# Optimization experiments

Measured on AMD Instinct MI355X. Metric: run time of the kernel, lower is better.

## Reference

```python
import jax, jax.numpy as jnp
import numpy as np

N = 100_000      # nodes
E = 3_200_000    # edges (avg degree 32)
F_IN = 64        # num_node_features
G = 256          # graphs in batch


def _lin(key, fan_in, fan_out):
    kw, kb = jax.random.split(key)
    bound = 1.0 / np.sqrt(fan_in)
    W = jax.random.uniform(kw, (fan_in, fan_out), jnp.float32, -bound, bound)
    b = jax.random.uniform(kb, (fan_out,), jnp.float32, -bound, bound)
    return W, b


def setup_inputs() -> dict:
    key = jax.random.key(0)
    ks = jax.random.split(key, 9)
    x = jax.random.normal(ks[0], (N, F_IN), jnp.float32)
    edge_index = jax.random.randint(ks[1], (2, E), 0, N, dtype=jnp.int64)
    batch = jnp.sort(jax.random.randint(ks[2], (N,), 0, G, dtype=jnp.int64))
    W1, b1 = _lin(ks[3], F_IN, 60)
    W2, b2 = _lin(ks[4], 60, 50)
    Wf1, bf1 = _lin(ks[5], 50, 30)
    Wf2, bf2 = _lin(ks[6], 30, 20)
    Wf3, bf3 = _lin(ks[7], 20, 10)
    Wo, bo = _lin(ks[8], 10, 1)
    return {"x": x, "edge_index": edge_index, "batch": batch,
            "W1": W1, "b1": b1, "W2": W2, "b2": b2,
            "Wf1": Wf1, "bf1": bf1, "Wf2": Wf2, "bf2": bf2,
            "Wf3": Wf3, "bf3": bf3, "Wo": Wo, "bo": bo}


def _gcn_norm(edge_index, n_nodes):
    # add self loops, then symmetric D^{-1/2} (A+I) D^{-1/2} edge weights
    loop = jnp.arange(n_nodes, dtype=edge_index.dtype)
    src = jnp.concatenate([edge_index[0], loop])
    dst = jnp.concatenate([edge_index[1], loop])
    deg = jax.ops.segment_sum(jnp.ones_like(dst, dtype=jnp.float32), dst,
                              num_segments=n_nodes)
    dinv = jax.lax.rsqrt(deg)  # deg >= 1 thanks to self loops
    norm = dinv[src] * dinv[dst]
    return src, dst, norm


def _gcn_conv(h, W, b, src, dst, norm, n_nodes):
    h = h @ W                                            # [N, out]
    msg = h[src] * norm[:, None]                         # gather over edges
    agg = jax.ops.segment_sum(msg, dst, num_segments=n_nodes)
    return agg + b


def reference(x, edge_index, batch, W1, b1, W2, b2,
              Wf1, bf1, Wf2, bf2, Wf3, bf3, Wo, bo):
    n_nodes = x.shape[0]
    src, dst, norm = _gcn_norm(edge_index, n_nodes)
    h = _gcn_conv(x, W1, b1, src, dst, norm, n_nodes)    # [N, 60]
    h = _gcn_conv(h, W2, b2, src, dst, norm, n_nodes)    # [N, 50]
    # global_add_pool over graph ids
    g = jax.ops.segment_sum(h, batch, num_segments=G)    # [G, 50]
    # MLP stack (no nonlinearities in the original forward)
    g = g @ Wf1 + bf1
    g = g @ Wf2 + bf2
    g = g @ Wf3 + bf3
    return g @ Wo + bo                                   # [G, 1]
```

## Files before the change

kernel.cpp:

```cpp
#include <hip/hip_runtime.h>


#define RSHIFT 7
#define RNODES 128
#define NB_MAX 1024
#define NBLK 512
#define STHREADS 512
#define STAGE_CAP 8192

__global__ void collapse_weights_k(
    const float* __restrict__ W1, const float* __restrict__ b1,
    const float* __restrict__ W2, const float* __restrict__ b2,
    const float* __restrict__ Wf1, const float* __restrict__ bf1,
    const float* __restrict__ Wf2, const float* __restrict__ bf2,
    const float* __restrict__ Wf3, const float* __restrict__ bf3,
    const float* __restrict__ Wo, const float* __restrict__ bo,
    float* __restrict__ w1c, float* __restrict__ sc)
{
    __shared__ float wo[10], w3[20], w2[30], w1[50], w2c[60];
    const int t = threadIdx.x;
    if (t < 10) wo[t] = Wo[t];
    __syncthreads();
    if (t < 20) { float s = 0.f; for (int j = 0; j < 10; ++j) s += Wf3[t*10+j]*wo[j]; w3[t] = s; }
    __syncthreads();
    if (t < 30) { float s = 0.f; for (int j = 0; j < 20; ++j) s += Wf2[t*20+j]*w3[j]; w2[t] = s; }
    __syncthreads();
    if (t < 50) { float s = 0.f; for (int j = 0; j < 30; ++j) s += Wf1[t*30+j]*w2[j]; w1[t] = s; }
    __syncthreads();
    if (t < 60) { float s = 0.f; for (int j = 0; j < 50; ++j) s += W2[t*50+j]*w1[j]; w2c[t] = s; }
    __syncthreads();
    { float s = 0.f; for (int j = 0; j < 60; ++j) s += W1[t*60+j]*w2c[j]; w1c[t] = s; }
    if (t == 0) {
        float c1 = 0.f; for (int j = 0; j < 60; ++j) c1 += b1[j]*w2c[j];
        float c2 = 0.f; for (int j = 0; j < 50; ++j) c2 += b2[j]*w1[j];
        float c0 = bo[0];
        for (int j = 0; j < 30; ++j) c0 += bf1[j]*w2[j];
        for (int j = 0; j < 20; ++j) c0 += bf2[j]*w3[j];
        for (int j = 0; j < 10; ++j) c0 += bf3[j]*wo[j];
        sc[0] = c1; sc[1] = c2; sc[2] = c0;
    }
}

__global__ void node_u_k(const float* __restrict__ x, const float* __restrict__ w1c,
                         float* __restrict__ u, int n) {
    int tid = blockIdx.x * blockDim.x + threadIdx.x;
    int wave = tid >> 6;
    int lane = threadIdx.x & 63;
    int node = wave * 4 + (lane >> 4);
    int sub = lane & 15;
    if (node >= n) return;
    float4 xv = *reinterpret_cast<const float4*>(x + (size_t)node * 64 + sub * 4);
    float4 wv = *reinterpret_cast<const float4*>(w1c + sub * 4);
    float val = xv.x * wv.x + xv.y * wv.y + xv.z * wv.z + xv.w * wv.w;
    val += __shfl_down(val, 8, 16);
    val += __shfl_down(val, 4, 16);
    val += __shfl_down(val, 2, 16);
    val += __shfl_down(val, 1, 16);
    if (sub == 0) u[node] = val;
}

__global__ void bin_count_k(const int* __restrict__ dst, int E, int chunk,
                            int nb, int* __restrict__ cnt_bm) {
    __shared__ int hist[NB_MAX];
    int tid = threadIdx.x;
    hist[tid] = 0; hist[tid + 512] = 0;
    __syncthreads();
    int e0 = blockIdx.x * chunk;
    int e1 = e0 + chunk; if (e1 > E) e1 = E;
    for (int j = 0; j < STAGE_CAP / (STHREADS * 4); ++j) {
        int i = e0 + tid * 4 + j * (STHREADS * 4);
        if (i + 3 < e1) {
            int4 d = *reinterpret_cast<const int4*>(dst + i);
            atomicAdd(&hist[d.x >> RSHIFT], 1);
            atomicAdd(&hist[d.y >> RSHIFT], 1);
            atomicAdd(&hist[d.z >> RSHIFT], 1);
            atomicAdd(&hist[d.w >> RSHIFT], 1);
        } else if (i < e1) {
            for (int k = i; k < e1; ++k) atomicAdd(&hist[dst[k] >> RSHIFT], 1);
        }
    }
    __syncthreads();
    for (int b = tid; b < nb; b += STHREADS)
        cnt_bm[(size_t)blockIdx.x * nb + b] = hist[b];
}

__global__ void scanA_k(const int* __restrict__ cnt_bm, int nb,
                        int* __restrict__ offs, int* __restrict__ total) {
    __shared__ int sums[STHREADS];
    int k = threadIdx.x, b = blockIdx.x;
    int v = cnt_bm[(size_t)k * nb + b];
    sums[k] = v;
    __syncthreads();
    for (int off = 1; off < STHREADS; off <<= 1) {
        int a = (k >= off) ? sums[k - off] : 0;
        __syncthreads();
        sums[k] += a;
        __syncthreads();
    }
    offs[(size_t)b * NBLK + k] = sums[k] - v;
    if (k == STHREADS - 1) total[b] = sums[k];
}

__global__ void scanB_k(const int* __restrict__ total, int nb,
                        int* __restrict__ base, int* __restrict__ endp,
                        const float* __restrict__ sc, float* __restrict__ out, int G) {
    __shared__ int sums[STHREADS];
    int t = threadIdx.x;
    if (t < G) out[t] = sc[2];
    int b0 = 2 * t, b1 = 2 * t + 1;
    int t0 = (b0 < nb) ? total[b0] : 0;
    int t1 = (b1 < nb) ? total[b1] : 0;
    int a0 = (t0 + 3) & ~3, a1 = (t1 + 3) & ~3;
    int pair = a0 + a1;
    sums[t] = pair;
    __syncthreads();
    for (int off = 1; off < STHREADS; off <<= 1) {
        int a = (t >= off) ? sums[t - off] : 0;
        __syncthreads();
        sums[t] += a;
        __syncthreads();
    }
    int excl = sums[t] - pair;
    if (b0 < nb) { base[b0] = excl; endp[b0] = excl + t0; }
    if (b1 < nb) { base[b1] = excl + a0; endp[b1] = excl + a0 + t1; }
}

__global__ void bin_scatter_k(const int* __restrict__ src, const int* __restrict__ dst,
                              int E, int chunk, int nb,
                              const int* __restrict__ base, const int* __restrict__ offs,
                              unsigned int* __restrict__ binned) {
    __shared__ int hist[NB_MAX];
    __shared__ int tbase[NB_MAX];
    __shared__ int adj[NB_MAX];
    __shared__ int sums[STHREADS];
    __shared__ unsigned int staged[STAGE_CAP];
    __shared__ unsigned short bof[STAGE_CAP];
    const int tid = threadIdx.x;
    hist[tid] = 0; hist[tid + 512] = 0;
    __syncthreads();
    int e0 = blockIdx.x * chunk;
    int e1 = e0 + chunk; if (e1 > E) e1 = E;
    const int QMAX = STAGE_CAP / (STHREADS * 4);
    unsigned int pk[QMAX * 4];
    int bk[QMAX * 4];
    int rk[QMAX * 4];
    int nv[QMAX];
    #pragma unroll
    for (int j = 0; j < QMAX; ++j) {
        int i = e0 + tid * 4 + j * (STHREADS * 4);
        int cnt = e1 - i; if (cnt > 4) cnt = 4; if (cnt < 0) cnt = 0;
        nv[j] = cnt;
        if (cnt == 4) {
            int4 s4 = *reinterpret_cast<const int4*>(src + i);
            int4 d4 = *reinterpret_cast<const int4*>(dst + i);
            pk[j*4+0] = (unsigned)s4.x | ((unsigned)(d4.x & (RNODES-1)) << 17);
            pk[j*4+1] = (unsigned)s4.y | ((unsigned)(d4.y & (RNODES-1)) << 17);
            pk[j*4+2] = (unsigned)s4.z | ((unsigned)(d4.z & (RNODES-1)) << 17);
            pk[j*4+3] = (unsigned)s4.w | ((unsigned)(d4.w & (RNODES-1)) << 17);
            bk[j*4+0] = d4.x >> RSHIFT; bk[j*4+1] = d4.y >> RSHIFT;
            bk[j*4+2] = d4.z >> RSHIFT; bk[j*4+3] = d4.w >> RSHIFT;
            rk[j*4+0] = atomicAdd(&hist[bk[j*4+0]], 1);
            rk[j*4+1] = atomicAdd(&hist[bk[j*4+1]], 1);
            rk[j*4+2] = atomicAdd(&hist[bk[j*4+2]], 1);
            rk[j*4+3] = atomicAdd(&hist[bk[j*4+3]], 1);
        } else {
            for (int l = 0; l < cnt; ++l) {
                int s = src[i + l], d = dst[i + l];
                pk[j*4+l] = (unsigned)s | ((unsigned)(d & (RNODES-1)) << 17);
                bk[j*4+l] = d >> RSHIFT;
                rk[j*4+l] = atomicAdd(&hist[bk[j*4+l]], 1);
            }
        }
    }
    __syncthreads();
    int h0 = hist[2*tid], h1 = hist[2*tid+1];
    int pair = h0 + h1;
    sums[tid] = pair;
    __syncthreads();
    for (int off = 1; off < STHREADS; off <<= 1) {
        int a = (tid >= off) ? sums[tid - off] : 0;
        __syncthreads();
        sums[tid] += a;
        __syncthreads();
    }
    int excl = sums[tid] - pair;
    tbase[2*tid] = excl;
    tbase[2*tid+1] = excl + h0;
    for (int b = 2*tid; b <= 2*tid+1; ++b)
        if (b < nb) adj[b] = base[b] + offs[(size_t)b * NBLK + blockIdx.x] - tbase[b];
    __syncthreads();
    #pragma unroll
    for (int j = 0; j < QMAX; ++j) {
        for (int l = 0; l < nv[j]; ++l) {
            int b = bk[j*4+l];
            int slot = tbase[b] + rk[j*4+l];
            staged[slot] = pk[j*4+l];
            bof[slot] = (unsigned short)b;
        }
    }
    __syncthreads();
    int tcount = e1 - e0;
    for (int s = tid; s < tcount; s += STHREADS) {
        int b = bof[s];
        binned[adj[b] + s] = staged[s];
    }
}

__global__ void degree_k(const unsigned int* __restrict__ binned, const int* __restrict__ base,
                         const int* __restrict__ endp, const float* __restrict__ u,
                         float* __restrict__ dinv, float* __restrict__ w, int n) {
    __shared__ int cnt[RNODES];
    int tid = threadIdx.x, b = blockIdx.x;
    if (tid < RNODES) cnt[tid] = 0;
    __syncthreads();
    int s0 = base[b], s1 = endp[b];
    int nvec = (s1 - s0) >> 2;
    for (int k = tid; k < nvec; k += blockDim.x) {
        uint4 p = *reinterpret_cast<const uint4*>(binned + s0 + 4 * k);
        atomicAdd(&cnt[p.x >> 17], 1);
        atomicAdd(&cnt[p.y >> 17], 1);
        atomicAdd(&cnt[p.z >> 17], 1);
        atomicAdd(&cnt[p.w >> 17], 1);
    }
    int i = s0 + 4 * nvec + tid;
    if (i < s1) atomicAdd(&cnt[binned[i] >> 17], 1);
    __syncthreads();
    int g = (b << RSHIFT) + tid;
    if (tid < RNODES && g < n) {
        float d = rsqrtf((float)(cnt[tid] + 1));
        dinv[g] = d;
        w[g] = d * u[g];
    }
}

__global__ void conv_mid_k(const unsigned int* __restrict__ binned, const int* __restrict__ base,
                           const int* __restrict__ endp,
                           const float* __restrict__ w, const float* __restrict__ dinv,
                           const float* __restrict__ u, const float* __restrict__ sc,
                           float* __restrict__ v, float* __restrict__ wb, int n) {
    __shared__ float acc[RNODES];
    int tid = threadIdx.x, b = blockIdx.x;
    if (tid < RNODES) acc[tid] = 0.f;
    __syncthreads();
    int s0 = base[b], s1 = endp[b];
    int nvec = (s1 - s0) >> 2;
    for (int k = tid; k < nvec; k += blockDim.x) {
        uint4 p = *reinterpret_cast<const uint4*>(binned + s0 + 4 * k);
        float wx = w[p.x & 0x1FFFF];
        float wy = w[p.y & 0x1FFFF];
        float wz = w[p.z & 0x1FFFF];
        float ww = w[p.w & 0x1FFFF];
        atomicAdd(&acc[p.x >> 17], wx);
        atomicAdd(&acc[p.y >> 17], wy);
        atomicAdd(&acc[p.z >> 17], wz);
        atomicAdd(&acc[p.w >> 17], ww);
    }
    int i = s0 + 4 * nvec + tid;
    if (i < s1) { unsigned p = binned[i]; atomicAdd(&acc[p >> 17], w[p & 0x1FFFF]); }
    __syncthreads();
    int g = (b << RSHIFT) + tid;
    if (tid < RNODES && g < n) {
        float di = dinv[g];
        float val = sc[0] + di * acc[tid] + di * di * u[g];
        v[g] = val;
        wb[g] = di * val;
    }
}

__global__ void conv_final_k(const unsigned int* __restrict__ binned, const int* __restrict__ base,
                             const int* __restrict__ endp,
                             const float* __restrict__ wb, const float* __restrict__ dinv,
                             const float* __restrict__ v, const float* __restrict__ sc,
                             const int* __restrict__ batch, float* __restrict__ out, int n) {
    __shared__ float acc[RNODES];
    __shared__ float tbuf[RNODES];
    __shared__ int gbuf[RNODES];
    int tid = threadIdx.x, b = blockIdx.x;
    if (tid < RNODES) acc[tid] = 0.f;
    __syncthreads();
    int s0 = base[b], s1 = endp[b];
    int nvec = (s1 - s0) >> 2;
    for (int k = tid; k < nvec; k += blockDim.x) {
        uint4 p = *reinterpret_cast<const uint4*>(binned + s0 + 4 * k);
        float wx = wb[p.x & 0x1FFFF];
        float wy = wb[p.y & 0x1FFFF];
        float wz = wb[p.z & 0x1FFFF];
        float ww = wb[p.w & 0x1FFFF];
        atomicAdd(&acc[p.x >> 17], wx);
        atomicAdd(&acc[p.y >> 17], wy);
        atomicAdd(&acc[p.z >> 17], wz);
        atomicAdd(&acc[p.w >> 17], ww);
    }
    int i = s0 + 4 * nvec + tid;
    if (i < s1) { unsigned p = binned[i]; atomicAdd(&acc[p >> 17], wb[p & 0x1FFFF]); }
    __syncthreads();
    int g = (b << RSHIFT) + tid;
    float tval = 0.f; int gid = -1;
    if (tid < RNODES && g < n) {
        float di = dinv[g];
        tval = sc[1] + di * acc[tid] + di * di * v[g];
        gid = batch[g];
    }
    if (tid < RNODES) { tbuf[tid] = tval; gbuf[tid] = gid; }
    __syncthreads();
    if (tid < RNODES && g < n) {
        bool head = (tid == 0) || (gbuf[tid - 1] != gid);
        if (head) {
            float s = 0.f;
            int i2 = tid;
            while (i2 < RNODES && gbuf[i2] == gid) { s += tbuf[i2]; ++i2; }
            atomicAdd(&out[gid], s);
        }
    }
}

extern "C" void kernel_launch(void* const* d_in, const int* in_sizes, int n_in,
                              void* d_out, int out_size, void* d_ws, size_t ws_size,
                              hipStream_t stream)
{
    const float* x    = (const float*)d_in[0];
    const int*   ei   = (const int*)d_in[1];
    const int*   batch= (const int*)d_in[2];
    const float* W1   = (const float*)d_in[3];
    const float* b1   = (const float*)d_in[4];
    const float* W2   = (const float*)d_in[5];
    const float* b2   = (const float*)d_in[6];
    const float* Wf1  = (const float*)d_in[7];
    const float* bf1  = (const float*)d_in[8];
    const float* Wf2  = (const float*)d_in[9];
    const float* bf2  = (const float*)d_in[10];
    const float* Wf3  = (const float*)d_in[11];
    const float* bf3  = (const float*)d_in[12];
    const float* Wo   = (const float*)d_in[13];
    const float* bo   = (const float*)d_in[14];
    float* out = (float*)d_out;

    const int n = in_sizes[0] / 64;
    const int E = in_sizes[1] / 2;
    const int G = out_size;
    const int* src = ei;
    const int* dst = ei + E;
    const int nb = (n + RNODES - 1) >> RSHIFT;

    float* ws_f = (float*)d_ws;
    int*   ws_i = (int*)d_ws;
    float* w1c    = ws_f;
    float* sc     = ws_f + 64;
    int*   basep  = ws_i + 128;
    int*   endp   = ws_i + 128 + NB_MAX;
    int*   total  = ws_i + 128 + 2*NB_MAX;
    int*   offs   = ws_i + 128 + 3*NB_MAX;
    size_t off_u  = 128 + 3*(size_t)NB_MAX + (size_t)nb * NBLK;
    off_u = (off_u + 3) & ~(size_t)3;
    float* u      = ws_f + off_u;
    float* dinv   = u + n;
    float* w      = dinv + n;
    float* v      = w + n;
    float* wb     = v + n;
    size_t off_b  = off_u + 5*(size_t)n;
    off_b = (off_b + 3) & ~(size_t)3;
    unsigned int* binned = (unsigned int*)(ws_f + off_b);
    int* cnt_bm = (int*)binned;

    int chunk = (E + NBLK - 1) / NBLK;
    chunk = (chunk + 3) & ~3;

    hipLaunchKernelGGL(collapse_weights_k, dim3(1), dim3(64), 0, stream,
                       W1, b1, W2, b2, Wf1, bf1, Wf2, bf2, Wf3, bf3, Wo, bo, w1c, sc);
    hipLaunchKernelGGL(node_u_k, dim3((n / 4 * 64 + 255) / 256 + 1), dim3(256), 0, stream,
                       x, w1c, u, n);
    hipLaunchKernelGGL(bin_count_k, dim3(NBLK), dim3(STHREADS), 0, stream,
                       dst, E, chunk, nb, cnt_bm);
    hipLaunchKernelGGL(scanA_k, dim3(nb), dim3(STHREADS), 0, stream,
                       cnt_bm, nb, offs, total);
    hipLaunchKernelGGL(scanB_k, dim3(1), dim3(STHREADS), 0, stream,
                       total, nb, basep, endp, sc, out, G);
    hipLaunchKernelGGL(bin_scatter_k, dim3(NBLK), dim3(STHREADS), 0, stream,
                       src, dst, E, chunk, nb, basep, offs, binned);
    hipLaunchKernelGGL(degree_k, dim3(nb), dim3(512), 0, stream,
                       binned, basep, endp, u, dinv, w, n);
    hipLaunchKernelGGL(conv_mid_k, dim3(nb), dim3(512), 0, stream,
                       binned, basep, endp, w, dinv, u, sc, v, wb, n);
    hipLaunchKernelGGL(conv_final_k, dim3(nb), dim3(512), 0, stream,
                       binned, basep, endp, wb, dinv, v, sc, batch, out, n);
}
```

Before: 204.4 us.

## Replace counting-sort passes with fixed-capacity bins and atomic cursors

Removes the separate bin-count pass and the two scan kernels by giving each destination bin a fixed capacity slot (BCAP) and reserving space with global atomic cursors in the scatter kernel. Node degrees are now computed with global atomics during scatter, replacing the degree pass over binned edges with a simple elementwise dinv kernel. This cuts a full read of dst and several launches, at the cost of global atomic contention and the assumption that no bin exceeds BCAP edges, which holds for uniform random graphs but would overflow on skewed degree distributions.

New measurement: 320.9 us. 1.57x slower.

```diff
diff --git a/kernel.cpp b/kernel.cpp
--- a/kernel.cpp
+++ b/kernel.cpp
@@ -7,6 +7,7 @@
 #define NBLK 512
 #define STHREADS 512
 #define STAGE_CAP 8192
+#define BCAP 6144
 
 __global__ void collapse_weights_k(
     const float* __restrict__ W1, const float* __restrict__ b1,
@@ -15,10 +16,12 @@
     const float* __restrict__ Wf2, const float* __restrict__ bf2,
     const float* __restrict__ Wf3, const float* __restrict__ bf3,
     const float* __restrict__ Wo, const float* __restrict__ bo,
-    float* __restrict__ w1c, float* __restrict__ sc)
+    float* __restrict__ w1c, float* __restrict__ sc,
+    int* __restrict__ cursor)
 {
     __shared__ float wo[10], w3[20], w2[30], w1[50], w2c[60];
     const int t = threadIdx.x;
+    for (int b = t; b < NB_MAX; b += 64) cursor[b] = 0;
     if (t < 10) wo[t] = Wo[t];
     __syncthreads();
     if (t < 20) { float s = 0.f; for (int j = 0; j < 10; ++j) s += Wf3[t*10+j]*wo[j]; w3[t] = s; }
@@ -42,13 +45,14 @@
 }
 
 __global__ void node_u_k(const float* __restrict__ x, const float* __restrict__ w1c,
-                         float* __restrict__ u, int n) {
+                         float* __restrict__ u, int* __restrict__ deg, int n) {
     int tid = blockIdx.x * blockDim.x + threadIdx.x;
     int wave = tid >> 6;
     int lane = threadIdx.x & 63;
     int node = wave * 4 + (lane >> 4);
     int sub = lane & 15;
     if (node >= n) return;
+    if (sub == 1) deg[node] = 0;
     float4 xv = *reinterpret_cast<const float4*>(x + (size_t)node * 64 + sub * 4);
     float4 wv = *reinterpret_cast<const float4*>(w1c + sub * 4);
     float val = xv.x * wv.x + xv.y * wv.y + xv.z * wv.z + xv.w * wv.w;
@@ -59,76 +63,10 @@
     if (sub == 0) u[node] = val;
 }
 
-__global__ void bin_count_k(const int* __restrict__ dst, int E, int chunk,
-                            int nb, int* __restrict__ cnt_bm) {
-    __shared__ int hist[NB_MAX];
-    int tid = threadIdx.x;
-    hist[tid] = 0; hist[tid + 512] = 0;
-    __syncthreads();
-    int e0 = blockIdx.x * chunk;
-    int e1 = e0 + chunk; if (e1 > E) e1 = E;
-    for (int j = 0; j < STAGE_CAP / (STHREADS * 4); ++j) {
-        int i = e0 + tid * 4 + j * (STHREADS * 4);
-        if (i + 3 < e1) {
-            int4 d = *reinterpret_cast<const int4*>(dst + i);
-            atomicAdd(&hist[d.x >> RSHIFT], 1);
-            atomicAdd(&hist[d.y >> RSHIFT], 1);
-            atomicAdd(&hist[d.z >> RSHIFT], 1);
-            atomicAdd(&hist[d.w >> RSHIFT], 1);
-        } else if (i < e1) {
-            for (int k = i; k < e1; ++k) atomicAdd(&hist[dst[k] >> RSHIFT], 1);
-        }
-    }
-    __syncthreads();
-    for (int b = tid; b < nb; b += STHREADS)
-        cnt_bm[(size_t)blockIdx.x * nb + b] = hist[b];
-}
-
-__global__ void scanA_k(const int* __restrict__ cnt_bm, int nb,
-                        int* __restrict__ offs, int* __restrict__ total) {
-    __shared__ int sums[STHREADS];
-    int k = threadIdx.x, b = blockIdx.x;
-    int v = cnt_bm[(size_t)k * nb + b];
-    sums[k] = v;
-    __syncthreads();
-    for (int off = 1; off < STHREADS; off <<= 1) {
-        int a = (k >= off) ? sums[k - off] : 0;
-        __syncthreads();
-        sums[k] += a;
-        __syncthreads();
-    }
-    offs[(size_t)b * NBLK + k] = sums[k] - v;
-    if (k == STHREADS - 1) total[b] = sums[k];
-}
-
-__global__ void scanB_k(const int* __restrict__ total, int nb,
-                        int* __restrict__ base, int* __restrict__ endp,
-                        const float* __restrict__ sc, float* __restrict__ out, int G) {
-    __shared__ int sums[STHREADS];
-    int t = threadIdx.x;
-    if (t < G) out[t] = sc[2];
-    int b0 = 2 * t, b1 = 2 * t + 1;
-    int t0 = (b0 < nb) ? total[b0] : 0;
-    int t1 = (b1 < nb) ? total[b1] : 0;
-    int a0 = (t0 + 3) & ~3, a1 = (t1 + 3) & ~3;
-    int pair = a0 + a1;
-    sums[t] = pair;
-    __syncthreads();
-    for (int off = 1; off < STHREADS; off <<= 1) {
-        int a = (t >= off) ? sums[t - off] : 0;
-        __syncthreads();
-        sums[t] += a;
-        __syncthreads();
-    }
-    int excl = sums[t] - pair;
-    if (b0 < nb) { base[b0] = excl; endp[b0] = excl + t0; }
-    if (b1 < nb) { base[b1] = excl + a0; endp[b1] = excl + a0 + t1; }
-}
-
-__global__ void bin_scatter_k(const int* __restrict__ src, const int* __restrict__ dst,
-                              int E, int chunk, int nb,
-                              const int* __restrict__ base, const int* __restrict__ offs,
-                              unsigned int* __restrict__ binned) {
+__global__ void scatter_k(const int* __restrict__ src, const int* __restrict__ dst,
+                          int E, int chunk, int nb,
+                          int* __restrict__ cursor, int* __restrict__ deg,
+                          unsigned int* __restrict__ binned) {
     __shared__ int hist[NB_MAX];
     __shared__ int tbase[NB_MAX];
     __shared__ int adj[NB_MAX];
@@ -153,6 +91,10 @@
         if (cnt == 4) {
             int4 s4 = *reinterpret_cast<const int4*>(src + i);
             int4 d4 = *reinterpret_cast<const int4*>(dst + i);
+            atomicAdd(&deg[d4.x], 1);
+            atomicAdd(&deg[d4.y], 1);
+            atomicAdd(&deg[d4.z], 1);
+            atomicAdd(&deg[d4.w], 1);
             pk[j*4+0] = (unsigned)s4.x | ((unsigned)(d4.x & (RNODES-1)) << 17);
             pk[j*4+1] = (unsigned)s4.y | ((unsigned)(d4.y & (RNODES-1)) << 17);
             pk[j*4+2] = (unsigned)s4.z | ((unsigned)(d4.z & (RNODES-1)) << 17);
@@ -166,6 +108,7 @@
         } else {
             for (int l = 0; l < cnt; ++l) {
                 int s = src[i + l], d = dst[i + l];
+                atomicAdd(&deg[d], 1);
                 pk[j*4+l] = (unsigned)s | ((unsigned)(d & (RNODES-1)) << 17);
                 bk[j*4+l] = d >> RSHIFT;
                 rk[j*4+l] = atomicAdd(&hist[bk[j*4+l]], 1);
@@ -186,8 +129,17 @@
     int excl = sums[tid] - pair;
     tbase[2*tid] = excl;
     tbase[2*tid+1] = excl + h0;
-    for (int b = 2*tid; b <= 2*tid+1; ++b)
-        if (b < nb) adj[b] = base[b] + offs[(size_t)b * NBLK + blockIdx.x] - tbase[b];
+    {
+        int b0 = 2*tid, b1 = 2*tid + 1;
+        if (b0 < nb && h0 > 0) {
+            int r = atomicAdd(&cursor[b0], h0);
+            adj[b0] = b0 * BCAP + r - excl;
+        }
+        if (b1 < nb && h1 > 0) {
+            int r = atomicAdd(&cursor[b1], h1);
+            adj[b1] = b1 * BCAP + r - (excl + h0);
+        }
+    }
     __syncthreads();
     #pragma unroll
     for (int j = 0; j < QMAX; ++j) {
@@ -206,35 +158,21 @@
     }
 }
 
-__global__ void degree_k(const unsigned int* __restrict__ binned, const int* __restrict__ base,
-                         const int* __restrict__ endp, const float* __restrict__ u,
-                         float* __restrict__ dinv, float* __restrict__ w, int n) {
-    __shared__ int cnt[RNODES];
-    int tid = threadIdx.x, b = blockIdx.x;
-    if (tid < RNODES) cnt[tid] = 0;
-    __syncthreads();
-    int s0 = base[b], s1 = endp[b];
-    int nvec = (s1 - s0) >> 2;
-    for (int k = tid; k < nvec; k += blockDim.x) {
-        uint4 p = *reinterpret_cast<const uint4*>(binned + s0 + 4 * k);
-        atomicAdd(&cnt[p.x >> 17], 1);
-        atomicAdd(&cnt[p.y >> 17], 1);
-        atomicAdd(&cnt[p.z >> 17], 1);
-        atomicAdd(&cnt[p.w >> 17], 1);
-    }
-    int i = s0 + 4 * nvec + tid;
-    if (i < s1) atomicAdd(&cnt[binned[i] >> 17], 1);
-    __syncthreads();
-    int g = (b << RSHIFT) + tid;
-    if (tid < RNODES && g < n) {
-        float d = rsqrtf((float)(cnt[tid] + 1));
+__global__ void dinv_w_k(const int* __restrict__ deg, const float* __restrict__ u,
+                         float* __restrict__ dinv, float* __restrict__ w,
+                         const float* __restrict__ sc, float* __restrict__ out,
+                         int n, int G) {
+    int g = blockIdx.x * blockDim.x + threadIdx.x;
+    if (g < G) out[g] = sc[2];
+    if (g < n) {
+        float d = rsqrtf((float)(deg[g] + 1));
         dinv[g] = d;
         w[g] = d * u[g];
     }
 }
 
-__global__ void conv_mid_k(const unsigned int* __restrict__ binned, const int* __restrict__ base,
-                           const int* __restrict__ endp,
+__global__ void conv_mid_k(const unsigned int* __restrict__ binned,
+                           const int* __restrict__ cursor,
                            const float* __restrict__ w, const float* __restrict__ dinv,
                            const float* __restrict__ u, const float* __restrict__ sc,
                            float* __restrict__ v, float* __restrict__ wb, int n) {
@@ -242,8 +180,9 @@
     int tid = threadIdx.x, b = blockIdx.x;
     if (tid < RNODES) acc[tid] = 0.f;
     __syncthreads();
-    int s0 = base[b], s1 = endp[b];
-    int nvec = (s1 - s0) >> 2;
+    int s0 = b * BCAP;
+    int cnt = cursor[b];
+    int nvec = cnt >> 2;
     for (int k = tid; k < nvec; k += blockDim.x) {
         uint4 p = *reinterpret_cast<const uint4*>(binned + s0 + 4 * k);
         float wx = w[p.x & 0x1FFFF];
@@ -255,8 +194,8 @@
         atomicAdd(&acc[p.z >> 17], wz);
         atomicAdd(&acc[p.w >> 17], ww);
     }
-    int i = s0 + 4 * nvec + tid;
-    if (i < s1) { unsigned p = binned[i]; atomicAdd(&acc[p >> 17], w[p & 0x1FFFF]); }
+    int i = 4 * nvec + tid;
+    if (i < cnt) { unsigned p = binned[s0 + i]; atomicAdd(&acc[p >> 17], w[p & 0x1FFFF]); }
     __syncthreads();
     int g = (b << RSHIFT) + tid;
     if (tid < RNODES && g < n) {
@@ -267,8 +206,8 @@
     }
 }
 
-__global__ void conv_final_k(const unsigned int* __restrict__ binned, const int* __restrict__ base,
-                             const int* __restrict__ endp,
+__global__ void conv_final_k(const unsigned int* __restrict__ binned,
+                             const int* __restrict__ cursor,
                              const float* __restrict__ wb, const float* __restrict__ dinv,
                              const float* __restrict__ v, const float* __restrict__ sc,
                              const int* __restrict__ batch, float* __restrict__ out, int n) {
@@ -278,8 +217,9 @@
     int tid = threadIdx.x, b = blockIdx.x;
     if (tid < RNODES) acc[tid] = 0.f;
     __syncthreads();
-    int s0 = base[b], s1 = endp[b];
-    int nvec = (s1 - s0) >> 2;
+    int s0 = b * BCAP;
+    int cnt = cursor[b];
+    int nvec = cnt >> 2;
     for (int k = tid; k < nvec; k += blockDim.x) {
         uint4 p = *reinterpret_cast<const uint4*>(binned + s0 + 4 * k);
         float wx = wb[p.x & 0x1FFFF];
@@ -291,8 +231,8 @@
         atomicAdd(&acc[p.z >> 17], wz);
         atomicAdd(&acc[p.w >> 17], ww);
     }
-    int i = s0 + 4 * nvec + tid;
-    if (i < s1) { unsigned p = binned[i]; atomicAdd(&acc[p >> 17], wb[p & 0x1FFFF]); }
+    int i = 4 * nvec + tid;
+    if (i < cnt) { unsigned p = binned[s0 + i]; atomicAdd(&acc[p >> 17], wb[p & 0x1FFFF]); }
     __syncthreads();
     int g = (b << RSHIFT) + tid;
     float tval = 0.f; int gid = -1;
@@ -346,11 +286,9 @@
     int*   ws_i = (int*)d_ws;
     float* w1c    = ws_f;
     float* sc     = ws_f + 64;
-    int*   basep  = ws_i + 128;
-    int*   endp   = ws_i + 128 + NB_MAX;
-    int*   total  = ws_i + 128 + 2*NB_MAX;
-    int*   offs   = ws_i + 128 + 3*NB_MAX;
-    size_t off_u  = 128 + 3*(size_t)NB_MAX + (size_t)nb * NBLK;
+    int*   cursor = ws_i + 128;
+    int*   deg    = ws_i + 128 + NB_MAX;
+    size_t off_u  = 128 + (size_t)NB_MAX + n;
     off_u = (off_u + 3) & ~(size_t)3;
     float* u      = ws_f + off_u;
     float* dinv   = u + n;
@@ -360,27 +298,21 @@
     size_t off_b  = off_u + 5*(size_t)n;
     off_b = (off_b + 3) & ~(size_t)3;
     unsigned int* binned = (unsigned int*)(ws_f + off_b);
-    int* cnt_bm = (int*)binned;
 
     int chunk = (E + NBLK - 1) / NBLK;
     chunk = (chunk + 3) & ~3;
 
     hipLaunchKernelGGL(collapse_weights_k, dim3(1), dim3(64), 0, stream,
-                       W1, b1, W2, b2, Wf1, bf1, Wf2, bf2, Wf3, bf3, Wo, bo, w1c, sc);
+                       W1, b1, W2, b2, Wf1, bf1, Wf2, bf2, Wf3, bf3, Wo, bo,
+                       w1c, sc, cursor);
     hipLaunchKernelGGL(node_u_k, dim3((n / 4 * 64 + 255) / 256 + 1), dim3(256), 0, stream,
-                       x, w1c, u, n);
-    hipLaunchKernelGGL(bin_count_k, dim3(NBLK), dim3(STHREADS), 0, stream,
-                       dst, E, chunk, nb, cnt_bm);
-    hipLaunchKernelGGL(scanA_k, dim3(nb), dim3(STHREADS), 0, stream,
-                       cnt_bm, nb, offs, total);
-    hipLaunchKernelGGL(scanB_k, dim3(1), dim3(STHREADS), 0, stream,
-                       total, nb, basep, endp, sc, out, G);
-    hipLaunchKernelGGL(bin_scatter_k, dim3(NBLK), dim3(STHREADS), 0, stream,
-                       src, dst, E, chunk, nb, basep, offs, binned);
-    hipLaunchKernelGGL(degree_k, dim3(nb), dim3(512), 0, stream,
-                       binned, basep, endp, u, dinv, w, n);
+                       x, w1c, u, deg, n);
+    hipLaunchKernelGGL(scatter_k, dim3(NBLK), dim3(STHREADS), 0, stream,
+                       src, dst, E, chunk, nb, cursor, deg, binned);
+    hipLaunchKernelGGL(dinv_w_k, dim3((n + 255) / 256), dim3(256), 0, stream,
+                       deg, u, dinv, w, sc, out, n, G);
     hipLaunchKernelGGL(conv_mid_k, dim3(nb), dim3(512), 0, stream,
-                       binned, basep, endp, w, dinv, u, sc, v, wb, n);
+                       binned, cursor, w, dinv, u, sc, v, wb, n);
     hipLaunchKernelGGL(conv_final_k, dim3(nb), dim3(512), 0, stream,
-                       binned, basep, endp, wb, dinv, v, sc, batch, out, n);
-}
+                       binned, cursor, wb, dinv, v, sc, batch, out, n);
+}
```
